# Kernel optimization log

Measured on AMD Instinct MI355X. Metric: run time of the kernel, lower is better.

Reference implementation:

```python
import jax, jax.numpy as jnp
import numpy as np

N, E, F, H, G = 50000, 640000, 128, 128, 64


def setup_inputs() -> dict:
    key = jax.random.key(0)
    ks = jax.random.split(key, 10)
    x = jax.random.normal(ks[0], (N, F), dtype=jnp.float32)
    edge_index = jax.random.randint(ks[1], (2, E), 0, N)
    batch = jnp.sort(jax.random.randint(ks[2], (N,), 0, G))

    def glorot(k, shp):
        return jax.random.normal(k, shp, dtype=jnp.float32) * np.float32(1.0 / np.sqrt(shp[0]))

    W1 = glorot(ks[3], (F, H)); b1 = jnp.zeros((H,), jnp.float32)
    W2 = glorot(ks[4], (H, H)); b2 = jnp.zeros((H,), jnp.float32)
    W3 = glorot(ks[5], (H, H)); b3 = jnp.zeros((H,), jnp.float32)
    W4 = glorot(ks[6], (H, 2)); b4 = jnp.zeros((2,), jnp.float32)
    return {"x": x, "W1": W1, "b1": b1, "W2": W2, "b2": b2,
            "W3": W3, "b3": b3, "W4": W4, "b4": b4,
            "edge_index": edge_index, "batch": batch, "num_graphs": G}


def reference(x, W1, b1, W2, b2, W3, b3, W4, b4, edge_index, batch, num_graphs):
    n = x.shape[0]
    loop = jnp.arange(n, dtype=edge_index.dtype)
    src = jnp.concatenate([edge_index[0], loop])  # with self-loops (PyG GCNConv default)
    dst = jnp.concatenate([edge_index[1], loop])
    # symmetric degree normalization: D^{-1/2} (A+I) D^{-1/2}
    deg = jax.ops.segment_sum(jnp.ones_like(src, dtype=x.dtype), dst, num_segments=n)
    dinv = jnp.where(deg > 0, jax.lax.rsqrt(deg), 0.0)
    norm = (dinv[src] * dinv[dst])[:, None]  # [E+N, 1]

    def gcn_conv(h, W, b):
        m = h @ W                                   # transform first (F->H), then propagate
        agg = jax.ops.segment_sum(m[src] * norm, dst, num_segments=n)
        return agg + b

    h = jax.nn.relu(gcn_conv(x, W1, b1))
    h = jax.nn.relu(gcn_conv(h, W2, b2))
    g = jax.ops.segment_max(h, batch, num_segments=num_graphs)  # global_max_pool
    z = jax.nn.relu(g @ W3 + b3)                    # dropout is identity in eval
    logits = z @ W4 + b4
    return jax.nn.log_softmax(logits, axis=1)
```

## Files before the change

### kernel.cpp

```cpp
#include <hip/hip_runtime.h>
#include <hip/hip_bf16.h>
#include <math.h>

#define HDIM 128
#define SCAN_B 256
#define NBLK 256

typedef short bfrag __attribute__((ext_vector_type(8)));
typedef float f32x4 __attribute__((ext_vector_type(4)));

__device__ inline unsigned short f2bf_rne(float x) {
    unsigned u = __float_as_uint(x);
    u = (u + 0x7fffu + ((u >> 16) & 1u)) >> 16;
    return (unsigned short)u;
}
__device__ inline float bf_lo(unsigned u) { return __uint_as_float(u << 16); }
__device__ inline float bf_hi(unsigned u) { return __uint_as_float(u & 0xffff0000u); }


__device__ inline void hist_body(int b, const int* __restrict__ dst,
                                 int* __restrict__ hist, int E, int chunk, int nbuck) {
    __shared__ int hl[256];
    int t = threadIdx.x;
    hl[t] = 0;
    __syncthreads();
    int start = b * chunk, end = min(E, start + chunk);
    for (int e = start + t; e < end; e += 256) atomicAdd(&hl[dst[e] >> 8], 1);
    __syncthreads();
    if (t < nbuck) hist[t * NBLK + b] = hl[t];
}

__device__ inline void wfrag_body(int b, const float* __restrict__ W1,
                                  const float* __restrict__ W2,
                                  unsigned short* __restrict__ w1h,
                                  unsigned short* __restrict__ w1l,
                                  unsigned short* __restrict__ w2h,
                                  unsigned short* __restrict__ w2l) {
    const float* W = (b < 64) ? W1 : W2;
    unsigned short* whi = (b < 64) ? w1h : w2h;
    unsigned short* wlo = (b < 64) ? w1l : w2l;
    int idx = (b & 63) * 256 + threadIdx.x;
    int k = idx >> 7;
    int n = idx & 127;
    int kt = k >> 5, q = (k >> 3) & 3, j = k & 7;
    int lm = n >> 3, nt = n & 7;
    int lane = q * 16 + lm;
    int o = ((kt * 8 + nt) * 64 + lane) * 8 + j;
    float x = W[idx];
    unsigned short hb = f2bf_rne(x);
    float hf = __uint_as_float(((unsigned)hb) << 16);
    unsigned short lb = f2bf_rne(x - hf);
    whi[o] = hb;
    wlo[o] = lb;
}

__device__ inline void scatter_body(int b, const int* __restrict__ srcv,
                                    const int* __restrict__ dstv,
                                    const int* __restrict__ hscan,
                                    int* __restrict__ sorted,
                                    int E, int chunk, int nbuck) {
    __shared__ int cur[256];
    int t = threadIdx.x;
    if (t < nbuck) cur[t] = hscan[t * NBLK + b];
    __syncthreads();
    int start = b * chunk, end = min(E, start + chunk);
    for (int e = start + t; e < end; e += 256) {
        int d = dstv[e];
        int pos = atomicAdd(&cur[d >> 8], 1);
        sorted[pos] = srcv[e] | ((d & 255) << 16);
    }
}

#define GBM 64
__device__ inline void gemm_f32_body(int b, const float* __restrict__ A,
                                     const unsigned short* __restrict__ whi,
                                     const unsigned short* __restrict__ wlo,
                                     unsigned short* __restrict__ C, int Nrows) {
    int tid = threadIdx.x;
    int w = tid >> 6, L = tid & 63;
    int lm = L & 15, lq = L >> 4;
    int row0 = b * GBM + w * 16;

    f32x4 acc[8];
#pragma unroll
    for (int nt = 0; nt < 8; ++nt) acc[nt] = (f32x4)(0.f);

#pragma unroll
    for (int kt = 0; kt < 4; ++kt) {
        int gr = row0 + lm;
        float4 v0 = make_float4(0.f, 0.f, 0.f, 0.f);
        float4 v1 = v0;
        if (gr < Nrows) {
            const float* p = &A[(size_t)gr * HDIM + kt * 32 + lq * 8];
            v0 = *(const float4*)p;
            v1 = *(const float4*)(p + 4);
        }
        float xv[8] = {v0.x, v0.y, v0.z, v0.w, v1.x, v1.y, v1.z, v1.w};
        bfrag ah, al;
#pragma unroll
        for (int j = 0; j < 8; ++j) {
            float x = xv[j];
            unsigned short hb = f2bf_rne(x);
            float hf = __uint_as_float(((unsigned)hb) << 16);
            unsigned short lb = f2bf_rne(x - hf);
            ah[j] = (short)hb;
            al[j] = (short)lb;
        }
#pragma unroll
        for (int nt = 0; nt < 8; ++nt) {
            int o = ((kt * 8 + nt) * 64 + L) * 8;
            bfrag wh = *(const bfrag*)&whi[o];
            bfrag wl = *(const bfrag*)&wlo[o];
            acc[nt] = __builtin_amdgcn_mfma_f32_16x16x32_bf16(ah, wh, acc[nt], 0, 0, 0);
            acc[nt] = __builtin_amdgcn_mfma_f32_16x16x32_bf16(al, wh, acc[nt], 0, 0, 0);
            acc[nt] = __builtin_amdgcn_mfma_f32_16x16x32_bf16(ah, wl, acc[nt], 0, 0, 0);
        }
    }

#pragma unroll
    for (int i = 0; i < 4; ++i) {
        int gr = row0 + lq * 4 + i;
        if (gr < Nrows) {
            bfrag e;
#pragma unroll
            for (int nt = 0; nt < 8; ++nt) e[nt] = (short)f2bf_rne(acc[nt][i]);
            *(bfrag*)&C[(size_t)gr * HDIM + lm * 8] = e;
        }
    }
}

__global__ __launch_bounds__(256) void mega1_kernel(const int* __restrict__ dst,
                                                    int* __restrict__ hist, int E,
                                                    int chunk, int nbuck,
                                                    const float* __restrict__ W1,
                                                    const float* __restrict__ W2,
                                                    unsigned short* __restrict__ w1h,
                                                    unsigned short* __restrict__ w1l,
                                                    unsigned short* __restrict__ w2h,
                                                    unsigned short* __restrict__ w2l) {
    int b = blockIdx.x;
    if (b < NBLK) hist_body(b, dst, hist, E, chunk, nbuck);
    else wfrag_body(b - NBLK, W1, W2, w1h, w1l, w2h, w2l);
}

__global__ __launch_bounds__(256) void mega3_kernel(const int* __restrict__ srcv,
                                                    const int* __restrict__ dstv,
                                                    const int* __restrict__ hscan,
                                                    int* __restrict__ sorted,
                                                    int E, int chunk, int nbuck,
                                                    const float* __restrict__ A,
                                                    const unsigned short* __restrict__ whi,
                                                    const unsigned short* __restrict__ wlo,
                                                    unsigned short* __restrict__ C, int Nrows) {
    int b = blockIdx.x;
    if (b < NBLK) scatter_body(b, srcv, dstv, hscan, sorted, E, chunk, nbuck);
    else gemm_f32_body(b - NBLK, A, whi, wlo, C, Nrows);
}

__global__ __launch_bounds__(SCAN_B) void scan1_kernel(const int* __restrict__ in,
                                                       int* __restrict__ out,
                                                       int* __restrict__ sums, int n) {
    __shared__ int s[SCAN_B];
    int t = threadIdx.x;
    int idx = blockIdx.x * SCAN_B + t;
    int v = (idx < n) ? in[idx] : 0;
    s[t] = v;
    __syncthreads();
    for (int off = 1; off < SCAN_B; off <<= 1) {
        int x = (t >= off) ? s[t - off] : 0;
        __syncthreads();
        s[t] += x;
        __syncthreads();
    }
    if (idx < n) out[idx] = s[t];
    if (t == SCAN_B - 1) sums[blockIdx.x] = s[t];
}

__global__ __launch_bounds__(SCAN_B) void scan3_kernel(const int* __restrict__ in,
                                                       int* __restrict__ out,
                                                       const int* __restrict__ sums,
                                                       int n, int nb) {
    __shared__ int s[SCAN_B];
    int t = threadIdx.x;
    int v = (t < nb) ? sums[t] : 0;
    s[t] = v;
    __syncthreads();
    for (int off = 1; off < SCAN_B; off <<= 1) {
        int x = (t >= off) ? s[t - off] : 0;
        __syncthreads();
        s[t] += x;
        __syncthreads();
    }
    int base = (blockIdx.x > 0) ? s[blockIdx.x - 1] : 0;
    int idx = blockIdx.x * SCAN_B + t;
    if (idx < n) out[idx] = out[idx] - in[idx] + base;
}

__global__ __launch_bounds__(256) void csr_kernel(const int* __restrict__ sorted,
                                                  const int* __restrict__ hscan,
                                                  int* __restrict__ rowstart,
                                                  float* __restrict__ dinv,
                                                  int* __restrict__ csr,
                                                  int N, int E, int nbuck) {
    __shared__ int cnt[256];
    __shared__ int s[256];
    __shared__ int cur[256];
    int b = blockIdx.x;
    int t = threadIdx.x;
    int start = hscan[b * NBLK];
    int end = (b + 1 < nbuck) ? hscan[(b + 1) * NBLK] : E;
    cnt[t] = 0;
    __syncthreads();
    for (int e = start + t; e < end; e += 256)
        atomicAdd(&cnt[(sorted[e] >> 16) & 255], 1);
    __syncthreads();
    int v = cnt[t];
    s[t] = v;
    __syncthreads();
    for (int off = 1; off < 256; off <<= 1) {
        int x = (t >= off) ? s[t - off] : 0;
        __syncthreads();
        s[t] += x;
        __syncthreads();
    }
    int excl = s[t] - v;
    int node = b * 256 + t;
    if (node < N) {
        rowstart[node] = start + excl;
        dinv[node] = rsqrtf((float)(v + 1));
    }
    if (b == nbuck - 1 && t == 0) rowstart[N] = E;
    cur[t] = start + excl;
    __syncthreads();
    for (int e = start + t; e < end; e += 256) {
        int ed = sorted[e];
        int pos = atomicAdd(&cur[(ed >> 16) & 255], 1);
        csr[pos] = ed & 0xFFFF;
    }
}

#define QACC(UV, WT)                                   \
    acc[0] = fmaf(WT, bf_lo((UV).x), acc[0]);          \
    acc[1] = fmaf(WT, bf_hi((UV).x), acc[1]);          \
    acc[2] = fmaf(WT, bf_lo((UV).y), acc[2]);          \
    acc[3] = fmaf(WT, bf_hi((UV).y), acc[3]);          \
    acc[4] = fmaf(WT, bf_lo((UV).z), acc[4]);          \
    acc[5] = fmaf(WT, bf_hi((UV).z), acc[5]);          \
    acc[6] = fmaf(WT, bf_lo((UV).w), acc[6]);          \
    acc[7] = fmaf(WT, bf_hi((UV).w), acc[7]);

__device__ inline void qgather(const uint4* __restrict__ m4,
                               const int* __restrict__ csr,
                               const float* __restrict__ dinv,
                               int p, int pend, int t, float* acc) {
    for (; p + 8 <= pend; p += 8) {
        int s0 = csr[p], s1 = csr[p + 1], s2 = csr[p + 2], s3 = csr[p + 3];
        int s4 = csr[p + 4], s5 = csr[p + 5], s6 = csr[p + 6], s7 = csr[p + 7];
        float w0 = dinv[s0], w1 = dinv[s1], w2 = dinv[s2], w3 = dinv[s3];
        float w4 = dinv[s4], w5 = dinv[s5], w6 = dinv[s6], w7 = dinv[s7];
        uint4 u0 = m4[(size_t)s0 * 16 + t];
        uint4 u1 = m4[(size_t)s1 * 16 + t];
        uint4 u2 = m4[(size_t)s2 * 16 + t];
        uint4 u3 = m4[(size_t)s3 * 16 + t];
        uint4 u4 = m4[(size_t)s4 * 16 + t];
        uint4 u5 = m4[(size_t)s5 * 16 + t];
        uint4 u6 = m4[(size_t)s6 * 16 + t];
        uint4 u7 = m4[(size_t)s7 * 16 + t];
        QACC(u0, w0); QACC(u1, w1); QACC(u2, w2); QACC(u3, w3);
        QACC(u4, w4); QACC(u5, w5); QACC(u6, w6); QACC(u7, w7);
    }
    if (p + 4 <= pend) {
        int s0 = csr[p], s1 = csr[p + 1], s2 = csr[p + 2], s3 = csr[p + 3];
        float w0 = dinv[s0], w1 = dinv[s1], w2 = dinv[s2], w3 = dinv[s3];
        uint4 u0 = m4[(size_t)s0 * 16 + t];
        uint4 u1 = m4[(size_t)s1 * 16 + t];
        uint4 u2 = m4[(size_t)s2 * 16 + t];
        uint4 u3 = m4[(size_t)s3 * 16 + t];
        QACC(u0, w0); QACC(u1, w1); QACC(u2, w2); QACC(u3, w3);
        p += 4;
    }
    if (p + 2 <= pend) {
        int s0 = csr[p], s1 = csr[p + 1];
        float w0 = dinv[s0], w1 = dinv[s1];
        uint4 u0 = m4[(size_t)s0 * 16 + t];
        uint4 u1 = m4[(size_t)s1 * 16 + t];
        QACC(u0, w0); QACC(u1, w1);
        p += 2;
    }
    if (p < pend) {
        int s0 = csr[p];
        float w0 = dinv[s0];
        uint4 u0 = m4[(size_t)s0 * 16 + t];
        QACC(u0, w0);
    }
}

__global__ __launch_bounds__(256) void agg_gemm_kernel(
        const uint4* __restrict__ m4,
        const int* __restrict__ rowstart,
        const int* __restrict__ csr,
        const float* __restrict__ dinv,
        const float* __restrict__ bias,
        const unsigned short* __restrict__ whi,
        const unsigned short* __restrict__ wlo,
        uint4* __restrict__ out_m, int n) {
    __shared__ float lds[16 * (HDIM + 4)];
    unsigned short* hbuf = (unsigned short*)lds;
    int t = threadIdx.x & 15;
    int nl = threadIdx.x >> 4;
    int node = blockIdx.x * 16 + nl;

    unsigned short hv[8] = {0, 0, 0, 0, 0, 0, 0, 0};
    if (node < n) {
        float dd = dinv[node];
        float acc[8];
        uint4 u = m4[(size_t)node * 16 + t];
        acc[0] = dd * bf_lo(u.x); acc[1] = dd * bf_hi(u.x);
        acc[2] = dd * bf_lo(u.y); acc[3] = dd * bf_hi(u.y);
        acc[4] = dd * bf_lo(u.z); acc[5] = dd * bf_hi(u.z);
        acc[6] = dd * bf_lo(u.w); acc[7] = dd * bf_hi(u.w);
        qgather(m4, csr, dinv, rowstart[node], rowstart[node + 1], t, acc);
        float4 b0 = *(const float4*)&bias[t * 8];
        float4 b1 = *(const float4*)&bias[t * 8 + 4];
        float bb[8] = {b0.x, b0.y, b0.z, b0.w, b1.x, b1.y, b1.z, b1.w};
#pragma unroll
        for (int j = 0; j < 8; ++j)
            hv[j] = f2bf_rne(fmaxf(fmaf(dd, acc[j], bb[j]), 0.f));
    }
    *(uint4*)&hbuf[nl * (HDIM + 8) + t * 8] = *(uint4*)hv;
    __syncthreads();

    int w = threadIdx.x >> 6, L = threadIdx.x & 63;
    int lm = L & 15, lq = L >> 4;
    f32x4 acc2[2];
    acc2[0] = (f32x4)(0.f);
    acc2[1] = (f32x4)(0.f);
#pragma unroll
    for (int kt = 0; kt < 4; ++kt) {
        bfrag a = *(const bfrag*)&hbuf[lm * (HDIM + 8) + kt * 32 + lq * 8];
#pragma unroll
        for (int q2 = 0; q2 < 2; ++q2) {
            int nt = w * 2 + q2;
            int o = ((kt * 8 + nt) * 64 + L) * 8;
            bfrag wh = *(const bfrag*)&whi[o];
            bfrag wl = *(const bfrag*)&wlo[o];
            acc2[q2] = __builtin_amdgcn_mfma_f32_16x16x32_bf16(a, wh, acc2[q2], 0, 0, 0);
            acc2[q2] = __builtin_amdgcn_mfma_f32_16x16x32_bf16(a, wl, acc2[q2], 0, 0, 0);
        }
    }
    __syncthreads();

    float* cbuf = lds;
#pragma unroll
    for (int q2 = 0; q2 < 2; ++q2) {
        int nt = w * 2 + q2;
#pragma unroll
        for (int i = 0; i < 4; ++i)
            cbuf[(lq * 4 + i) * (HDIM + 4) + lm * 8 + nt] = acc2[q2][i];
    }
    __syncthreads();

    if (node < n) {
        float4 r0 = *(const float4*)&cbuf[nl * (HDIM + 4) + t * 8];
        float4 r1 = *(const float4*)&cbuf[nl * (HDIM + 4) + t * 8 + 4];
        unsigned short ev[8];
        ev[0] = f2bf_rne(r0.x); ev[1] = f2bf_rne(r0.y);
        ev[2] = f2bf_rne(r0.z); ev[3] = f2bf_rne(r0.w);
        ev[4] = f2bf_rne(r1.x); ev[5] = f2bf_rne(r1.y);
        ev[6] = f2bf_rne(r1.z); ev[7] = f2bf_rne(r1.w);
        out_m[(size_t)node * 16 + t] = *(uint4*)ev;
    }
}

__global__ __launch_bounds__(256) void agg_pool_kernel(const uint4* __restrict__ m4,
                                                       const int* __restrict__ rowstart,
                                                       const int* __restrict__ csr,
                                                       const float* __restrict__ dinv,
                                                       const float* __restrict__ bias,
                                                       const int* __restrict__ batch,
                                                       unsigned int* __restrict__ g, int n) {
    __shared__ float smx[16][HDIM];
    __shared__ int sgid[16];
    int t = threadIdx.x & 15;
    int nl = threadIdx.x >> 4;
    int node = blockIdx.x * 16 + nl;
    bool valid = node < n;
    if (valid) {
        float dd = dinv[node];
        float acc[8];
        uint4 u = m4[(size_t)node * 16 + t];
        acc[0] = dd * bf_lo(u.x); acc[1] = dd * bf_hi(u.x);
        acc[2] = dd * bf_lo(u.y); acc[3] = dd * bf_hi(u.y);
        acc[4] = dd * bf_lo(u.z); acc[5] = dd * bf_hi(u.z);
        acc[6] = dd * bf_lo(u.w); acc[7] = dd * bf_hi(u.w);
        qgather(m4, csr, dinv, rowstart[node], rowstart[node + 1], t, acc);
        float4 b0 = *(const float4*)&bias[t * 8];
        float4 b1 = *(const float4*)&bias[t * 8 + 4];
        float4 r0, r1;
        r0.x = fmaxf(fmaf(dd, acc[0], b0.x), 0.f);
        r0.y = fmaxf(fmaf(dd, acc[1], b0.y), 0.f);
        r0.z = fmaxf(fmaf(dd, acc[2], b0.z), 0.f);
        r0.w = fmaxf(fmaf(dd, acc[3], b0.w), 0.f);
        r1.x = fmaxf(fmaf(dd, acc[4], b1.x), 0.f);
        r1.y = fmaxf(fmaf(dd, acc[5], b1.y), 0.f);
        r1.z = fmaxf(fmaf(dd, acc[6], b1.z), 0.f);
        r1.w = fmaxf(fmaf(dd, acc[7], b1.w), 0.f);
        *(float4*)&smx[nl][t * 8] = r0;
        *(float4*)&smx[nl][t * 8 + 4] = r1;
    }
    if (t == 0) sgid[nl] = valid ? batch[node] : -1;
    __syncthreads();
    if (threadIdx.x < HDIM) {
        int c = threadIdx.x;
        int curg = -1;
        float run = 0.f;
#pragma unroll
        for (int r = 0; r < 16; ++r) {
            int gg = sgid[r];
            if (gg < 0) continue;
            if (gg != curg) {
                if (curg >= 0) atomicMax(&g[curg * HDIM + c], __float_as_uint(run));
                curg = gg;
                run = smx[r][c];
            } else {
                run = fmaxf(run, smx[r][c]);
            }
        }
        if (curg >= 0) atomicMax(&g[curg * HDIM + c], __float_as_uint(run));
    }
}

__global__ __launch_bounds__(128) void mlp_kernel(const unsigned int* __restrict__ gbits,
                                                  const float* __restrict__ W3,
                                                  const float* __restrict__ b3,
                                                  const float* __restrict__ W4,
                                                  const float* __restrict__ b4,
                                                  float* __restrict__ out) {
    __shared__ float gs[HDIM];
    __shared__ float r0[HDIM];
    __shared__ float r1[HDIM];
    int j = threadIdx.x;
    int b = blockIdx.x;
    gs[j] = __uint_as_float(gbits[b * HDIM + j]);
    __syncthreads();
    float acc = b3[j];
#pragma unroll 8
    for (int k = 0; k < HDIM; ++k) acc = fmaf(gs[k], W3[k * HDIM + j], acc);
    float z = fmaxf(acc, 0.f);
    r0[j] = z * W4[j * 2 + 0];
    r1[j] = z * W4[j * 2 + 1];
    __syncthreads();
    for (int off = 64; off > 0; off >>= 1) {
        if (j < off) {
            r0[j] += r0[j + off];
            r1[j] += r1[j + off];
        }
        __syncthreads();
    }
    if (j == 0) {
        float l0 = r0[0] + b4[0];
        float l1 = r1[0] + b4[1];
        float mx = fmaxf(l0, l1);
        float lse = mx + logf(expf(l0 - mx) + expf(l1 - mx));
        out[b * 2 + 0] = l0 - lse;
        out[b * 2 + 1] = l1 - lse;
    }
}

extern "C" void kernel_launch(void* const* d_in, const int* in_sizes, int n_in,
                              void* d_out, int out_size, void* d_ws, size_t ws_size,
                              hipStream_t stream) {
    const float* x  = (const float*)d_in[0];
    const float* W1 = (const float*)d_in[1];
    const float* b1 = (const float*)d_in[2];
    const float* W2 = (const float*)d_in[3];
    const float* b2 = (const float*)d_in[4];
    const float* W3 = (const float*)d_in[5];
    const float* b3 = (const float*)d_in[6];
    const float* W4 = (const float*)d_in[7];
    const float* b4 = (const float*)d_in[8];
    const int* ei    = (const int*)d_in[9];
    const int* batch = (const int*)d_in[10];

    const int N = in_sizes[0] / HDIM;
    const int E = in_sizes[9] / 2;
    const int G = out_size / 2;
    const int* src = ei;
    const int* dst = ei + E;

    const int nbuck = (N + 255) >> 8;
    const int nscan = nbuck * NBLK;
    const int chunk = (E + NBLK - 1) / NBLK;

    const int Nr = ((N + 63) / 64) * 64;
    char* wsb = (char*)d_ws;
    size_t o = 0;
    unsigned int* g = (unsigned int*)(wsb + o); o += (size_t)G * HDIM * 4;
    size_t zero_bytes = o;
    int* hist = (int*)(wsb + o);           o += (size_t)nscan * 4;
    int* hscan = (int*)(wsb + o);          o += (size_t)nscan * 4;
    int* sums = (int*)(wsb + o);           o += 256 * 4;
    int* rowstart = (int*)(wsb + o);       o += (size_t)(Nr + 64) * 4;
    float* dinv = (float*)(wsb + o);       o += (size_t)Nr * 4;
    int* sorted = (int*)(wsb + o);         o += (size_t)E * 4;
    int* csr = (int*)(wsb + o);            o += (size_t)E * 4;
    unsigned short* wf1h = (unsigned short*)(wsb + o); o += (size_t)HDIM * HDIM * 2;
    unsigned short* wf1l = (unsigned short*)(wsb + o); o += (size_t)HDIM * HDIM * 2;
    unsigned short* wf2h = (unsigned short*)(wsb + o); o += (size_t)HDIM * HDIM * 2;
    unsigned short* wf2l = (unsigned short*)(wsb + o); o += (size_t)HDIM * HDIM * 2;
    unsigned short* m = (unsigned short*)(wsb + o);    o += (size_t)Nr * HDIM * 2;
    unsigned short* m2 = (unsigned short*)(wsb + o);   o += (size_t)Nr * HDIM * 2;
    (void)ws_size; (void)n_in;

    (void)hipMemsetAsync(d_ws, 0, zero_bytes, stream);

    int sblocks = (nscan + SCAN_B - 1) / SCAN_B;
    int gemm_blocks = (N + GBM - 1) / GBM;
    int agg_blocks = (N + 15) / 16;

    mega1_kernel<<<NBLK + 128, 256, 0, stream>>>(dst, hist, E, chunk, nbuck,
                                                 W1, W2, wf1h, wf1l, wf2h, wf2l);
    scan1_kernel<<<sblocks, SCAN_B, 0, stream>>>(hist, hscan, sums, nscan);
    scan3_kernel<<<sblocks, SCAN_B, 0, stream>>>(hist, hscan, sums, nscan, sblocks);
    mega3_kernel<<<NBLK + gemm_blocks, 256, 0, stream>>>(src, dst, hscan, sorted,
                                                         E, chunk, nbuck,
                                                         x, wf1h, wf1l, m, N);
    csr_kernel<<<nbuck, 256, 0, stream>>>(sorted, hscan, rowstart, dinv, csr, N, E, nbuck);
    agg_gemm_kernel<<<agg_blocks, 256, 0, stream>>>((const uint4*)m, rowstart, csr,
                                                    dinv, b1, wf2h, wf2l,
                                                    (uint4*)m2, N);
    agg_pool_kernel<<<agg_blocks, 256, 0, stream>>>((const uint4*)m2, rowstart, csr,
                                                    dinv, b2, batch, g, N);
    mlp_kernel<<<G, 128, 0, stream>>>(g, W3, b3, W4, b4, (float*)d_out);
}
```

Baseline: 202.8 us.

## Fuse graph-build kernels into one cooperative kernel with grid syncs

Replaces the five launches for histogram, weight fragmenting, two scan passes, scatter and CSR build with a single cooperative kernel of 512 blocks that separates the phases with grid-wide syncs. The layer-1 GEMM tiles are spread across the scan and scatter phases so they run on blocks that would otherwise sit idle. The aim is to cut launch gaps and the serialization of the small scan kernels. In exchange it adds grid-sync overhead, ties occupancy to a fixed grid (launch bounds 256,2), and falls back to the old launch sequence if the cooperative launch fails.

```diff
diff --git a/kernel.cpp b/kernel.cpp
--- a/kernel.cpp
+++ b/kernel.cpp
@@ -1,10 +1,14 @@
 #include <hip/hip_runtime.h>
 #include <hip/hip_bf16.h>
+#include <hip/hip_cooperative_groups.h>
 #include <math.h>
+
+namespace cg = cooperative_groups;
 
 #define HDIM 128
 #define SCAN_B 256
 #define NBLK 256
+#define CGRID 512
 
 typedef short bfrag __attribute__((ext_vector_type(8)));
 typedef float f32x4 __attribute__((ext_vector_type(4)));
@@ -54,6 +58,43 @@
     wlo[o] = lb;
 }
 
+__device__ inline void scan1_body(int b, const int* __restrict__ in,
+                                  int* __restrict__ out, int* __restrict__ sums, int n) {
+    __shared__ int s1[SCAN_B];
+    int t = threadIdx.x;
+    int idx = b * SCAN_B + t;
+    int v = (idx < n) ? in[idx] : 0;
+    s1[t] = v;
+    __syncthreads();
+    for (int off = 1; off < SCAN_B; off <<= 1) {
+        int x = (t >= off) ? s1[t - off] : 0;
+        __syncthreads();
+        s1[t] += x;
+        __syncthreads();
+    }
+    if (idx < n) out[idx] = s1[t];
+    if (t == SCAN_B - 1) sums[b] = s1[t];
+}
+
+__device__ inline void scan3_body(int b, const int* __restrict__ in,
+                                  int* __restrict__ out, const int* __restrict__ sums,
+                                  int n, int nb) {
+    __shared__ int s3[SCAN_B];
+    int t = threadIdx.x;
+    int v = (t < nb) ? sums[t] : 0;
+    s3[t] = v;
+    __syncthreads();
+    for (int off = 1; off < SCAN_B; off <<= 1) {
+        int x = (t >= off) ? s3[t - off] : 0;
+        __syncthreads();
+        s3[t] += x;
+        __syncthreads();
+    }
+    int base = (b > 0) ? s3[b - 1] : 0;
+    int idx = b * SCAN_B + t;
+    if (idx < n) out[idx] = out[idx] - in[idx] + base;
+}
+
 __device__ inline void scatter_body(int b, const int* __restrict__ srcv,
                                     const int* __restrict__ dstv,
                                     const int* __restrict__ hscan,
@@ -68,6 +109,48 @@
         int d = dstv[e];
         int pos = atomicAdd(&cur[d >> 8], 1);
         sorted[pos] = srcv[e] | ((d & 255) << 16);
+    }
+}
+
+__device__ inline void csr_body(int b, const int* __restrict__ sorted,
+                                const int* __restrict__ hscan,
+                                int* __restrict__ rowstart,
+                                float* __restrict__ dinv,
+                                int* __restrict__ csr,
+                                int N, int E, int nbuck) {
+    __shared__ int ccnt[256];
+    __shared__ int cs[256];
+    __shared__ int ccur[256];
+    int t = threadIdx.x;
+    int start = hscan[b * NBLK];
+    int end = (b + 1 < nbuck) ? hscan[(b + 1) * NBLK] : E;
+    ccnt[t] = 0;
+    __syncthreads();
+    for (int e = start + t; e < end; e += 256)
+        atomicAdd(&ccnt[(sorted[e] >> 16) & 255], 1);
+    __syncthreads();
+    int v = ccnt[t];
+    cs[t] = v;
+    __syncthreads();
+    for (int off = 1; off < 256; off <<= 1) {
+        int x = (t >= off) ? cs[t - off] : 0;
+        __syncthreads();
+        cs[t] += x;
+        __syncthreads();
+    }
+    int excl = cs[t] - v;
+    int node = b * 256 + t;
+    if (node < N) {
+        rowstart[node] = start + excl;
+        dinv[node] = rsqrtf((float)(v + 1));
+    }
+    if (b == nbuck - 1 && t == 0) rowstart[N] = E;
+    ccur[t] = start + excl;
+    __syncthreads();
+    for (int e = start + t; e < end; e += 256) {
+        int ed = sorted[e];
+        int pos = atomicAdd(&ccur[(ed >> 16) & 255], 1);
+        csr[pos] = ed & 0xFFFF;
     }
 }
 
@@ -127,6 +210,52 @@
             *(bfrag*)&C[(size_t)gr * HDIM + lm * 8] = e;
         }
     }
+}
+
+__global__ __launch_bounds__(256, 2) void build_kernel(
+        const int* src, const int* dst, int E, int chunk, int nbuck, int nscan,
+        int sblocks, int N, int gb,
+        const float* W1, const float* W2,
+        unsigned short* w1h, unsigned short* w1l,
+        unsigned short* w2h, unsigned short* w2l,
+        int* hist, int* hscan, int* sums,
+        int* sorted, int* rowstart, float* dinv, int* csr,
+        const float* x, unsigned short* m) {
+    cg::grid_group grid = cg::this_grid();
+    int b = blockIdx.x;
+    int t2 = (gb + 2) / 3;
+    int t3 = min(gb, 2 * t2);
+
+    if (b < NBLK) hist_body(b, dst, hist, E, chunk, nbuck);
+    else if (b < NBLK + 128) wfrag_body(b - NBLK, W1, W2, w1h, w1l, w2h, w2l);
+    __threadfence();
+    grid.sync();
+
+    if (b < sblocks) scan1_body(b, hist, hscan, sums, nscan);
+    else {
+        for (int tile = b - sblocks; tile < t2; tile += CGRID - sblocks)
+            gemm_f32_body(tile, x, w1h, w1l, m, N);
+    }
+    __threadfence();
+    grid.sync();
+
+    if (b < sblocks) scan3_body(b, hist, hscan, sums, nscan, sblocks);
+    else {
+        for (int tile = t2 + (b - sblocks); tile < t3; tile += CGRID - sblocks)
+            gemm_f32_body(tile, x, w1h, w1l, m, N);
+    }
+    __threadfence();
+    grid.sync();
+
+    if (b < NBLK) scatter_body(b, src, dst, hscan, sorted, E, chunk, nbuck);
+    else {
+        for (int tile = t3 + (b - NBLK); tile < gb; tile += CGRID - NBLK)
+            gemm_f32_body(tile, x, w1h, w1l, m, N);
+    }
+    __threadfence();
+    grid.sync();
+
+    if (b < nbuck) csr_body(b, sorted, hscan, rowstart, dinv, csr, N, E, nbuck);
 }
 
 __global__ __launch_bounds__(256) void mega1_kernel(const int* __restrict__ dst,
@@ -143,6 +272,19 @@
     else wfrag_body(b - NBLK, W1, W2, w1h, w1l, w2h, w2l);
 }
 
+__global__ __launch_bounds__(SCAN_B) void scan1_kernel(const int* __restrict__ in,
+                                                       int* __restrict__ out,
+                                                       int* __restrict__ sums, int n) {
+    scan1_body(blockIdx.x, in, out, sums, n);
+}
+
+__global__ __launch_bounds__(SCAN_B) void scan3_kernel(const int* __restrict__ in,
+                                                       int* __restrict__ out,
+                                                       const int* __restrict__ sums,
+                                                       int n, int nb) {
+    scan3_body(blockIdx.x, in, out, sums, n, nb);
+}
+
 __global__ __launch_bounds__(256) void mega3_kernel(const int* __restrict__ srcv,
                                                     const int* __restrict__ dstv,
                                                     const int* __restrict__ hscan,
@@ -157,86 +299,13 @@
     else gemm_f32_body(b - NBLK, A, whi, wlo, C, Nrows);
 }
 
-__global__ __launch_bounds__(SCAN_B) void scan1_kernel(const int* __restrict__ in,
-                                                       int* __restrict__ out,
-                                                       int* __restrict__ sums, int n) {
-    __shared__ int s[SCAN_B];
-    int t = threadIdx.x;
-    int idx = blockIdx.x * SCAN_B + t;
-    int v = (idx < n) ? in[idx] : 0;
-    s[t] = v;
-    __syncthreads();
-    for (int off = 1; off < SCAN_B; off <<= 1) {
-        int x = (t >= off) ? s[t - off] : 0;
-        __syncthreads();
-        s[t] += x;
-        __syncthreads();
-    }
-    if (idx < n) out[idx] = s[t];
-    if (t == SCAN_B - 1) sums[blockIdx.x] = s[t];
-}
-
-__global__ __launch_bounds__(SCAN_B) void scan3_kernel(const int* __restrict__ in,
-                                                       int* __restrict__ out,
-                                                       const int* __restrict__ sums,
-                                                       int n, int nb) {
-    __shared__ int s[SCAN_B];
-    int t = threadIdx.x;
-    int v = (t < nb) ? sums[t] : 0;
-    s[t] = v;
-    __syncthreads();
-    for (int off = 1; off < SCAN_B; off <<= 1) {
-        int x = (t >= off) ? s[t - off] : 0;
-        __syncthreads();
-        s[t] += x;
-        __syncthreads();
-    }
-    int base = (blockIdx.x > 0) ? s[blockIdx.x - 1] : 0;
-    int idx = blockIdx.x * SCAN_B + t;
-    if (idx < n) out[idx] = out[idx] - in[idx] + base;
-}
-
 __global__ __launch_bounds__(256) void csr_kernel(const int* __restrict__ sorted,
                                                   const int* __restrict__ hscan,
                                                   int* __restrict__ rowstart,
                                                   float* __restrict__ dinv,
                                                   int* __restrict__ csr,
                                                   int N, int E, int nbuck) {
-    __shared__ int cnt[256];
-    __shared__ int s[256];
-    __shared__ int cur[256];
-    int b = blockIdx.x;
-    int t = threadIdx.x;
-    int start = hscan[b * NBLK];
-    int end = (b + 1 < nbuck) ? hscan[(b + 1) * NBLK] : E;
-    cnt[t] = 0;
-    __syncthreads();
-    for (int e = start + t; e < end; e += 256)
-        atomicAdd(&cnt[(sorted[e] >> 16) & 255], 1);
-    __syncthreads();
-    int v = cnt[t];
-    s[t] = v;
-    __syncthreads();
-    for (int off = 1; off < 256; off <<= 1) {
-        int x = (t >= off) ? s[t - off] : 0;
-        __syncthreads();
-        s[t] += x;
-        __syncthreads();
-    }
-    int excl = s[t] - v;
-    int node = b * 256 + t;
-    if (node < N) {
-        rowstart[node] = start + excl;
-        dinv[node] = rsqrtf((float)(v + 1));
-    }
-    if (b == nbuck - 1 && t == 0) rowstart[N] = E;
-    cur[t] = start + excl;
-    __syncthreads();
-    for (int e = start + t; e < end; e += 256) {
-        int ed = sorted[e];
-        int pos = atomicAdd(&cur[(ed >> 16) & 255], 1);
-        csr[pos] = ed & 0xFFFF;
-    }
+    csr_body(blockIdx.x, sorted, hscan, rowstart, dinv, csr, N, E, nbuck);
 }
 
 #define QACC(UV, WT)                                   \
@@ -518,14 +587,30 @@
     int gemm_blocks = (N + GBM - 1) / GBM;
     int agg_blocks = (N + 15) / 16;
 
-    mega1_kernel<<<NBLK + 128, 256, 0, stream>>>(dst, hist, E, chunk, nbuck,
-                                                 W1, W2, wf1h, wf1l, wf2h, wf2l);
-    scan1_kernel<<<sblocks, SCAN_B, 0, stream>>>(hist, hscan, sums, nscan);
-    scan3_kernel<<<sblocks, SCAN_B, 0, stream>>>(hist, hscan, sums, nscan, sblocks);
-    mega3_kernel<<<NBLK + gemm_blocks, 256, 0, stream>>>(src, dst, hscan, sorted,
-                                                         E, chunk, nbuck,
-                                                         x, wf1h, wf1l, m, N);
-    csr_kernel<<<nbuck, 256, 0, stream>>>(sorted, hscan, rowstart, dinv, csr, N, E, nbuck);
+    hipError_t cerr;
+    {
+        void* kargs[] = {
+            (void*)&src, (void*)&dst, (void*)&E, (void*)&chunk, (void*)&nbuck,
+            (void*)&nscan, (void*)&sblocks, (void*)&N, (void*)&gemm_blocks,
+            (void*)&W1, (void*)&W2,
+            (void*)&wf1h, (void*)&wf1l, (void*)&wf2h, (void*)&wf2l,
+            (void*)&hist, (void*)&hscan, (void*)&sums,
+            (void*)&sorted, (void*)&rowstart, (void*)&dinv, (void*)&csr,
+            (void*)&x, (void*)&m};
+        cerr = hipLaunchCooperativeKernel((void*)build_kernel, dim3(CGRID), dim3(256),
+                                          kargs, 0, stream);
+    }
+    if (cerr != hipSuccess) {
+        mega1_kernel<<<NBLK + 128, 256, 0, stream>>>(dst, hist, E, chunk, nbuck,
+                                                     W1, W2, wf1h, wf1l, wf2h, wf2l);
+        scan1_kernel<<<sblocks, SCAN_B, 0, stream>>>(hist, hscan, sums, nscan);
+        scan3_kernel<<<sblocks, SCAN_B, 0, stream>>>(hist, hscan, sums, nscan, sblocks);
+        mega3_kernel<<<NBLK + gemm_blocks, 256, 0, stream>>>(src, dst, hscan, sorted,
+                                                             E, chunk, nbuck,
+                                                             x, wf1h, wf1l, m, N);
+        csr_kernel<<<nbuck, 256, 0, stream>>>(sorted, hscan, rowstart, dinv, csr,
+                                              N, E, nbuck);
+    }
     agg_gemm_kernel<<<agg_blocks, 256, 0, stream>>>((const uint4*)m, rowstart, csr,
                                                     dinv, b1, wf2h, wf2l,
                                                     (uint4*)m2, N);
```

After: 682.1 us. +236.4%, slower.
